# Performance work log

Hardware: AMD Instinct MI355X
Metric: run time of the kernel (lower is better)

## Reference

```python
import jax, jax.numpy as jnp
import numpy as np

C_QKV = 1024
C_HIDDEN = 64
NUM_HEADS = 16
INF = 1e9


def setup_inputs() -> dict:
    key = jax.random.key(0)
    ks = jax.random.split(key, 10)
    B, S = 2, 2048
    d = C_QKV
    hd = C_HIDDEN * NUM_HEADS
    sc = 0.02
    return {
        "input_qkv": jax.random.normal(ks[0], (B, S, d), jnp.float32),
        "mask": jnp.ones((B, 1, 1, S), jnp.float32),
        "bias": jax.random.normal(ks[1], (1, NUM_HEADS, S, S), jnp.float32) * sc,
        "wq": jax.random.normal(ks[2], (d, hd), jnp.float32) * sc,
        "wk": jax.random.normal(ks[3], (d, hd), jnp.float32) * sc,
        "wv": jax.random.normal(ks[4], (d, hd), jnp.float32) * sc,
        "wg": jax.random.normal(ks[5], (d, hd), jnp.float32) * sc,
        "bg": jnp.zeros((hd,), jnp.float32),
        "wo": jax.random.normal(ks[6], (hd, d), jnp.float32) * sc,
        "bo": jnp.zeros((d,), jnp.float32),
    }


def reference(input_qkv, mask, bias, wq, wk, wv, wg, bg, wo, bo):
    B, S, _ = input_qkv.shape
    H, C = NUM_HEADS, C_HIDDEN
    # projections -> [B, H, S, C]
    q = (input_qkv @ wq).reshape(B, S, H, C).transpose(0, 2, 1, 3)
    k = (input_qkv @ wk).reshape(B, S, H, C).transpose(0, 2, 1, 3)
    v = (input_qkv @ wv).reshape(B, S, H, C).transpose(0, 2, 1, 3)
    q = q / jnp.asarray(C, q.dtype) ** 0.5
    # scores [B, H, S, S] with additive mask and pair bias
    a = jnp.einsum("bhqc,bhkc->bhqk", q, k)
    a = a + (mask - 1.0) * INF + bias
    a = jax.nn.softmax(a, axis=-1)
    o = jnp.einsum("bhqk,bhkc->bhqc", a, v).transpose(0, 2, 1, 3)  # [B,S,H,C]
    gate = jax.nn.sigmoid(input_qkv @ wg + bg).reshape(B, S, H, C)
    o = (o * gate).reshape(B, S, H * C)
    return o @ wo + bo
```

## Files before the change

kernel.cpp:

```cpp
#include <hip/hip_runtime.h>
#include <hip/hip_bf16.h>
#include <stdint.h>

typedef unsigned short u16;
typedef __attribute__((ext_vector_type(8))) short short8;
typedef __attribute__((ext_vector_type(4))) short short4v;
typedef __attribute__((ext_vector_type(4))) float f32x4;

#define MFMA16 __builtin_amdgcn_mfma_f32_16x16x32_bf16

#define GLOAD_LDS16(gsrc, ldst) \
  __builtin_amdgcn_global_load_lds((const __attribute__((address_space(1))) void*)(gsrc), \
                                   (__attribute__((address_space(3))) void*)(ldst), 16, 0, 0)

__device__ __forceinline__ u16 f2bf(float x) {
  union { float f; uint32_t u; } v; v.f = x;
  uint32_t r = v.u + 0x7FFFu + ((v.u >> 16) & 1u);
  return (u16)(r >> 16);
}
__device__ __forceinline__ u16 f2bf_rn(float x) {
  __hip_bfloat16 h = __float2bfloat16(x);
  return *reinterpret_cast<u16*>(&h);
}
__device__ __forceinline__ float bf2f(u16 b) {
  union { uint32_t u; float f; } v; v.u = ((uint32_t)b) << 16;
  return v.f;
}

__global__ __launch_bounds__(256) void convert_bf16_kernel(
    const float* __restrict__ in, u16* __restrict__ out, int n) {
  int i = (blockIdx.x * 256 + threadIdx.x) * 8;
  if (i >= n) return;
  float4 a = *(const float4*)(in + i);
  float4 b = *(const float4*)(in + i + 4);
  short8 t;
  t[0] = (short)f2bf(a.x); t[1] = (short)f2bf(a.y);
  t[2] = (short)f2bf(a.z); t[3] = (short)f2bf(a.w);
  t[4] = (short)f2bf(b.x); t[5] = (short)f2bf(b.y);
  t[6] = (short)f2bf(b.z); t[7] = (short)f2bf(b.w);
  *(short8*)(out + i) = t;
}

__global__ __launch_bounds__(256) void transpose_w64_4(
    const float* __restrict__ w0, const float* __restrict__ w1,
    const float* __restrict__ w2, const float* __restrict__ w3,
    u16* __restrict__ WT) {
  __shared__ float tile[64][68];
  const int t = threadIdx.x;
  const int z = blockIdx.z;
  const float* W = (z == 0) ? w0 : (z == 1) ? w1 : (z == 2) ? w2 : w3;
  u16* dst_base = WT + (size_t)z * 1024 * 1024;
  const int k0 = blockIdx.x * 64, n0 = blockIdx.y * 64;
  {
    int r = t >> 2, c0 = (t & 3) * 16;
    const float* src = W + (size_t)(k0 + r) * 1024 + n0 + c0;
#pragma unroll
    for (int j = 0; j < 16; j += 4) {
      float4 v = *(const float4*)(src + j);
      tile[r][c0 + j + 0] = v.x; tile[r][c0 + j + 1] = v.y;
      tile[r][c0 + j + 2] = v.z; tile[r][c0 + j + 3] = v.w;
    }
  }
  __syncthreads();
  {
    int n = t >> 2, kq = (t & 3) * 16;
    short8 t0, t1;
#pragma unroll
    for (int j = 0; j < 8; ++j)  t0[j] = (short)f2bf(tile[kq + j][n]);
#pragma unroll
    for (int j = 0; j < 8; ++j)  t1[j] = (short)f2bf(tile[kq + 8 + j][n]);
    u16* dst = dst_base + (size_t)(n0 + n) * 1024 + k0 + kq;
    *(short8*)dst = t0;
    *(short8*)(dst + 8) = t1;
  }
}

__global__ __launch_bounds__(256) void transpose_w64(
    const float* __restrict__ W, u16* __restrict__ WT, int KK, int NN) {
  __shared__ float tile[64][68];
  const int t = threadIdx.x;
  const int k0 = blockIdx.x * 64, n0 = blockIdx.y * 64;
  {
    int r = t >> 2, c0 = (t & 3) * 16;
    const float* src = W + (size_t)(k0 + r) * NN + n0 + c0;
#pragma unroll
    for (int j = 0; j < 16; j += 4) {
      float4 v = *(const float4*)(src + j);
      tile[r][c0 + j + 0] = v.x; tile[r][c0 + j + 1] = v.y;
      tile[r][c0 + j + 2] = v.z; tile[r][c0 + j + 3] = v.w;
    }
  }
  __syncthreads();
  {
    int n = t >> 2, kq = (t & 3) * 16;
    short8 t0, t1;
#pragma unroll
    for (int j = 0; j < 8; ++j)  t0[j] = (short)f2bf(tile[kq + j][n]);
#pragma unroll
    for (int j = 0; j < 8; ++j)  t1[j] = (short)f2bf(tile[kq + 8 + j][n]);
    u16* dst = WT + (size_t)(n0 + n) * KK + k0 + kq;
    *(short8*)dst = t0;
    *(short8*)(dst + 8) = t1;
  }
}

__global__ __launch_bounds__(256) void transpose_v64(
    const u16* __restrict__ vin, u16* __restrict__ vout) {
  __shared__ u16 tile[64][80];
  const int t = threadIdx.x;
  const int s0 = blockIdx.x * 64;
  const int bh = blockIdx.y;
  const int b = bh >> 4, h = bh & 15;
  {
    int r = t >> 2, c0 = (t & 3) * 16;
    const u16* src = vin + (size_t)(b * 2048 + s0 + r) * 1024 + h * 64 + c0;
    *(short8*)&tile[r][c0] = *(const short8*)src;
    *(short8*)&tile[r][c0 + 8] = *(const short8*)(src + 8);
  }
  __syncthreads();
  {
    int c = t >> 2, s4 = (t & 3) * 16;
    short8 t0, t1;
#pragma unroll
    for (int j = 0; j < 8; ++j) t0[j] = (short)tile[s4 + j][c];
#pragma unroll
    for (int j = 0; j < 8; ++j) t1[j] = (short)tile[s4 + 8 + j][c];
    u16* dst = vout + (size_t)(bh * 64 + c) * 2048 + s0 + s4;
    *(short8*)dst = t0;
    *(short8*)(dst + 8) = t1;
  }
}

__global__ __launch_bounds__(256) void gemm_bt128(
    const u16* __restrict__ A, const u16* __restrict__ BTbase,
    void* __restrict__ dstbase, const float* __restrict__ bvec, int mode) {
  const int K = 1024;
  const int tid = threadIdx.x, lane = tid & 63, w = tid >> 6;
  const int wr = w >> 1, wc = w & 1;
  const int l15 = lane & 15, lg = lane >> 4;
  const int z = (mode < 0) ? (int)blockIdx.z : mode;
  const u16* BT = (mode < 0) ? BTbase + (size_t)z * 1024 * 1024 : BTbase;
  const int rbase = blockIdx.x * 128;
  const int nbase = blockIdx.y * 128;
  __shared__ u16 lsA[128 * 64];
  __shared__ u16 lsB[128 * 64];
  f32x4 acc[4][4] = {};
  const int col8 = (lane & 7) * 8;
  for (int kt = 0; kt < K / 64; ++kt) {
#pragma unroll
    for (int i = 0; i < 4; ++i) {
      int row = w * 32 + i * 8 + (lane >> 3);
      const u16* sa = A + (size_t)(rbase + row) * K + kt * 64 + col8;
      GLOAD_LDS16(sa, lsA + (w * 32 + i * 8) * 64 + lane * 8);
      const u16* sb = BT + (size_t)(nbase + row) * K + kt * 64 + col8;
      GLOAD_LDS16(sb, lsB + (w * 32 + i * 8) * 64 + lane * 8);
    }
    __syncthreads();
#pragma unroll
    for (int kk = 0; kk < 2; ++kk) {
      short8 af[4], bfr[4];
#pragma unroll
      for (int m = 0; m < 4; ++m)
        af[m] = *(const short8*)&lsA[(wr * 64 + m * 16 + l15) * 64 + kk * 32 + lg * 8];
#pragma unroll
      for (int n = 0; n < 4; ++n)
        bfr[n] = *(const short8*)&lsB[(wc * 64 + n * 16 + l15) * 64 + kk * 32 + lg * 8];
#pragma unroll
      for (int m = 0; m < 4; ++m)
#pragma unroll
        for (int n = 0; n < 4; ++n)
          acc[m][n] = MFMA16(af[m], bfr[n], acc[m][n], 0, 0, 0);
    }
    __syncthreads();
  }
  const int r0 = rbase + wr * 64;
  const int c0 = nbase + wc * 64;
  if (z == 4) {
    float* out = (float*)dstbase;
#pragma unroll
    for (int m = 0; m < 4; ++m)
#pragma unroll
      for (int n = 0; n < 4; ++n)
#pragma unroll
        for (int i = 0; i < 4; ++i) {
          int r = r0 + m * 16 + lg * 4 + i;
          int c = c0 + n * 16 + l15;
          out[(size_t)r * 1024 + c] = acc[m][n][i] + bvec[c];
        }
  } else {
    u16* dq = (u16*)dstbase + (size_t)z * 4096 * 1024;
#pragma unroll
    for (int m = 0; m < 4; ++m)
#pragma unroll
      for (int n = 0; n < 4; ++n)
#pragma unroll
        for (int i = 0; i < 4; ++i) {
          int r = r0 + m * 16 + lg * 4 + i;
          int c = c0 + n * 16 + l15;
          float v = acc[m][n][i];
          if (z == 0) v *= 0.125f;
          else if (z == 3) v = 1.f / (1.f + __expf(-(v + bvec[c])));
          dq[(size_t)r * 1024 + c] = f2bf(v);
        }
  }
}

__global__ __launch_bounds__(512, 2) void attn_kernel(
    const u16* __restrict__ qws, const u16* __restrict__ kws,
    const u16* __restrict__ vt, const u16* __restrict__ gws,
    const float* __restrict__ bias, const float* __restrict__ mask,
    u16* __restrict__ og) {
  const int tid = threadIdx.x;
  const int lane = tid & 63;
  const int w = tid >> 6;
  const int bb = w >> 2;
  const int ws = w & 3;
  const int l15 = lane & 15, lg = lane >> 4;
  const int qt = blockIdx.x;
  const int h = blockIdx.y;
  const int kb0 = ((h << 1) | (qt >> 3)) & 31;

#define KWIN(KB) (((KB) + kb0) & 31)

  __shared__ __align__(16) u16 ring[3][16384];
  __shared__ __align__(16) u16 lsP[8][2304];
  __shared__ __align__(16) u16 lsM[4096];

  const float* bias_base = bias + ((size_t)h * 2048 + qt * 128) * 2048;
  const u16* k_base0 = kws + (size_t)h * 64;
  const u16* k_base1 = kws + (size_t)2048 * 1024 + h * 64;
  const u16* vt_base0 = vt + (size_t)(h * 64) * 2048;
  const u16* vt_base1 = vt + (size_t)((16 + h) * 64) * 2048;

  {
    float4 m0 = *(const float4*)(mask + tid * 8);
    float4 m1 = *(const float4*)(mask + tid * 8 + 4);
    short8 mm;
    mm[0] = (short)f2bf((m0.x - 1.f) * 1e9f); mm[1] = (short)f2bf((m0.y - 1.f) * 1e9f);
    mm[2] = (short)f2bf((m0.z - 1.f) * 1e9f); mm[3] = (short)f2bf((m0.w - 1.f) * 1e9f);
    mm[4] = (short)f2bf((m1.x - 1.f) * 1e9f); mm[5] = (short)f2bf((m1.y - 1.f) * 1e9f);
    mm[6] = (short)f2bf((m1.z - 1.f) * 1e9f); mm[7] = (short)f2bf((m1.w - 1.f) * 1e9f);
    *(short8*)&lsM[tid * 8] = mm;
  }

  const size_t qrow0 = (size_t)(bb * 2048 + qt * 128 + ws * 32 + l15) * 1024 + h * 64;
  const size_t qrow1 = qrow0 + 16 * 1024;
  short8 qf00 = *(const short8*)(qws + qrow0 + lg * 8);
  short8 qf01 = *(const short8*)(qws + qrow0 + 32 + lg * 8);
  short8 qf10 = *(const short8*)(qws + qrow1 + lg * 8);
  short8 qf11 = *(const short8*)(qws + qrow1 + 32 + lg * 8);
  asm volatile("" :: "v"(qf00), "v"(qf01), "v"(qf10), "v"(qf11));
  asm volatile("s_waitcnt vmcnt(0)" ::: "memory");
  __builtin_amdgcn_sched_barrier(0);

  f32x4 O[2][4] = {};
  float lacc0 = 0.f, lacc1 = 0.f;
  f32x4 bA0, bA1, bA2, bA3, bA4, bA5, bA6, bA7;
  f32x4 bB0, bB1, bB2, bB3, bB4, bB5, bB6, bB7;
  f32x4 kX0, kX1, vX0, vX1, kY0, kY1, vY0, vY1;

#define STAGE_ISSUE(K0, K1, V0, V1, KB) {                                           \
    int kw_ = KWIN(KB);                                                             \
    int r_ = tid >> 3, cg_ = tid & 7;                                               \
    const u16* kp0 = k_base0 + (size_t)(kw_ * 64 + r_) * 1024 + cg_ * 8;            \
    const u16* kp1 = k_base1 + (size_t)(kw_ * 64 + r_) * 1024 + cg_ * 8;            \
    const u16* vp0 = vt_base0 + (size_t)r_ * 2048 + kw_ * 64 + cg_ * 8;             \
    const u16* vp1 = vt_base1 + (size_t)r_ * 2048 + kw_ * 64 + cg_ * 8;             \
    asm volatile("global_load_dwordx4 %0, %1, off" : "=v"(K0) : "v"(kp0));          \
    asm volatile("global_load_dwordx4 %0, %1, off" : "=v"(K1) : "v"(kp1));          \
    asm volatile("global_load_dwordx4 %0, %1, off" : "=v"(V0) : "v"(vp0));          \
    asm volatile("global_load_dwordx4 %0, %1, off" : "=v"(V1) : "v"(vp1));          \
  }

#define STAGE_WRITE(SLOT, K0, K1, V0, V1) {                                         \
    int r_ = tid >> 3, cg_ = tid & 7;                                               \
    int d0_ = (r_ * 8 + (cg_ ^ (r_ & 7))) * 8;                                      \
    *(f32x4*)&ring[SLOT][d0_] = K0;                                                 \
    *(f32x4*)&ring[SLOT][4096 + d0_] = V0;                                          \
    *(f32x4*)&ring[SLOT][8192 + d0_] = K1;                                          \
    *(f32x4*)&ring[SLOT][12288 + d0_] = V1;                                         \
  }

#define BIAS_ISSUE(R0, R1, R2, R3, R4, R5, R6, R7, KB) {                            \
    const float* bp_ = bias_base + (size_t)(ws * 32 + l15) * 2048 + KWIN(KB) * 64 + lg * 4; \
    asm volatile("global_load_dwordx4 %0, %1, off" : "=v"(R0) : "v"(bp_));          \
    asm volatile("global_load_dwordx4 %0, %1, off" : "=v"(R1) : "v"(bp_ + 16));     \
    asm volatile("global_load_dwordx4 %0, %1, off" : "=v"(R2) : "v"(bp_ + 32));     \
    asm volatile("global_load_dwordx4 %0, %1, off" : "=v"(R3) : "v"(bp_ + 48));     \
    asm volatile("global_load_dwordx4 %0, %1, off" : "=v"(R4) : "v"(bp_ + 16 * 2048)); \
    asm volatile("global_load_dwordx4 %0, %1, off" : "=v"(R5) : "v"(bp_ + 16 * 2048 + 16)); \
    asm volatile("global_load_dwordx4 %0, %1, off" : "=v"(R6) : "v"(bp_ + 16 * 2048 + 32)); \
    asm volatile("global_load_dwordx4 %0, %1, off" : "=v"(R7) : "v"(bp_ + 16 * 2048 + 48)); \
  }

#define COMPUTE(SLOT, KB, X0, X1, X2, X3, X4, X5, X6, X7) {                         \
    const u16* Kc_ = &ring[SLOT][bb * 8192];                                        \
    const u16* Vc_ = &ring[SLOT][bb * 8192 + 4096];                                 \
    f32x4 bb0_[4] = {X0, X1, X2, X3};                                               \
    f32x4 bb1_[4] = {X4, X5, X6, X7};                                               \
    f32x4 s_[2][4];                                                                 \
    _Pragma("unroll") for (int kt = 0; kt < 4; ++kt) {                              \
      int krow_ = kt * 16 + l15;                                                    \
      int sw_ = krow_ & 7;                                                          \
      short8 kfa_ = *(const short8*)&Kc_[(krow_ * 8 + (lg ^ sw_)) * 8];             \
      short8 kfb_ = *(const short8*)&Kc_[(krow_ * 8 + ((4 + lg) ^ sw_)) * 8];       \
      short4v mk_ = *(const short4v*)&lsM[bb * 2048 + KWIN(KB) * 64 + kt * 16 + lg * 4]; \
      f32x4 ci0_, ci1_;                                                             \
      _Pragma("unroll") for (int i = 0; i < 4; ++i) {                               \
        float m_ = bf2f((u16)mk_[i]);                                               \
        ci0_[i] = bb0_[kt][i] + m_;                                                 \
        ci1_[i] = bb1_[kt][i] + m_;                                                 \
      }                                                                             \
      s_[0][kt] = MFMA16(kfa_, qf00, ci0_, 0, 0, 0);                                \
      s_[0][kt] = MFMA16(kfb_, qf01, s_[0][kt], 0, 0, 0);                           \
      s_[1][kt] = MFMA16(kfa_, qf10, ci1_, 0, 0, 0);                                \
      s_[1][kt] = MFMA16(kfb_, qf11, s_[1][kt], 0, 0, 0);                           \
    }                                                                               \
    _Pragma("unroll") for (int kt = 0; kt < 4; ++kt) {                              \
      short4v p0_, p1_;                                                             \
      _Pragma("unroll") for (int i = 0; i < 4; ++i) {                               \
        float e0_ = __expf(s_[0][kt][i]); lacc0 += e0_; p0_[i] = (short)f2bf_rn(e0_); \
        float e1_ = __expf(s_[1][kt][i]); lacc1 += e1_; p1_[i] = (short)f2bf_rn(e1_); \
      }                                                                             \
      *(short4v*)&lsP[w][(l15) * 72 + kt * 16 + lg * 4] = p0_;                      \
      *(short4v*)&lsP[w][(16 + l15) * 72 + kt * 16 + lg * 4] = p1_;                 \
    }                                                                               \
    short8 pf00_ = *(const short8*)&lsP[w][(l15) * 72 + lg * 8];                    \
    short8 pf01_ = *(const short8*)&lsP[w][(l15) * 72 + 32 + lg * 8];               \
    short8 pf10_ = *(const short8*)&lsP[w][(16 + l15) * 72 + lg * 8];               \
    short8 pf11_ = *(const short8*)&lsP[w][(16 + l15) * 72 + 32 + lg * 8];          \
    _Pragma("unroll") for (int cf = 0; cf < 4; ++cf) {                              \
      int c_ = cf * 16 + l15;                                                       \
      int sw_ = c_ & 7;                                                             \
      short8 vf0_ = *(const short8*)&Vc_[(c_ * 8 + (lg ^ sw_)) * 8];                \
      short8 vf1_ = *(const short8*)&Vc_[(c_ * 8 + ((4 + lg) ^ sw_)) * 8];          \
      O[0][cf] = MFMA16(vf0_, pf00_, O[0][cf], 0, 0, 0);                            \
      O[0][cf] = MFMA16(vf1_, pf01_, O[0][cf], 0, 0, 0);                            \
      O[1][cf] = MFMA16(vf0_, pf10_, O[1][cf], 0, 0, 0);                            \
      O[1][cf] = MFMA16(vf1_, pf11_, O[1][cf], 0, 0, 0);                            \
    } }

#define BODY(KB, N, ISK0, ISK1, ISV0, ISV1, WRK0, WRK1, WRV0, WRV1,                 \
             X0, X1, X2, X3, X4, X5, X6, X7) {                                      \
    if ((KB) + 2 < 32) STAGE_ISSUE(ISK0, ISK1, ISV0, ISV1, (KB) + 2);               \
    COMPUTE((KB) % 3, KB, X0, X1, X2, X3, X4, X5, X6, X7);                          \
    if ((KB) + 2 < 32) BIAS_ISSUE(X0, X1, X2, X3, X4, X5, X6, X7, (KB) + 2);        \
    asm volatile("s_waitcnt vmcnt(" #N ")" ::: "memory");                           \
    __builtin_amdgcn_sched_barrier(0);                                              \
    if ((KB) + 1 < 32) {                                                            \
      STAGE_WRITE(((KB) + 1) % 3, WRK0, WRK1, WRV0, WRV1);                          \
      asm volatile("s_waitcnt lgkmcnt(0)" ::: "memory");                            \
      __builtin_amdgcn_sched_barrier(0);                                            \
      __builtin_amdgcn_s_barrier();                                                 \
    } }

  STAGE_ISSUE(kX0, kX1, vX0, vX1, 0);
  BIAS_ISSUE(bA0, bA1, bA2, bA3, bA4, bA5, bA6, bA7, 0);
  STAGE_ISSUE(kY0, kY1, vY0, vY1, 1);
  BIAS_ISSUE(bB0, bB1, bB2, bB3, bB4, bB5, bB6, bB7, 1);
  asm volatile("s_waitcnt vmcnt(12)" ::: "memory");
  __builtin_amdgcn_sched_barrier(0);
  STAGE_WRITE(0, kX0, kX1, vX0, vX1);
  asm volatile("s_waitcnt lgkmcnt(0)" ::: "memory");
  __builtin_amdgcn_sched_barrier(0);
  __builtin_amdgcn_s_barrier();

  for (int kb2 = 0; kb2 < 30; kb2 += 2) {
    BODY(kb2,     12, kX0, kX1, vX0, vX1, kY0, kY1, vY0, vY1,
         bA0, bA1, bA2, bA3, bA4, bA5, bA6, bA7);
    BODY(kb2 + 1, 12, kY0, kY1, vY0, vY1, kX0, kX1, vX0, vX1,
         bB0, bB1, bB2, bB3, bB4, bB5, bB6, bB7);
  }
  BODY(30, 0, kX0, kX1, vX0, vX1, kY0, kY1, vY0, vY1,
       bA0, bA1, bA2, bA3, bA4, bA5, bA6, bA7);
  BODY(31, 0, kY0, kY1, vY0, vY1, kX0, kX1, vX0, vX1,
       bB0, bB1, bB2, bB3, bB4, bB5, bB6, bB7);

  lacc0 += __shfl_xor(lacc0, 16); lacc0 += __shfl_xor(lacc0, 32);
  lacc1 += __shfl_xor(lacc1, 16); lacc1 += __shfl_xor(lacc1, 32);
  {
    float inv0 = 1.f / lacc0, inv1 = 1.f / lacc1;
#pragma unroll
    for (int cf = 0; cf < 4; ++cf) {
      short4v ga = *(const short4v*)(gws + qrow0 + cf * 16 + lg * 4);
      short4v gb = *(const short4v*)(gws + qrow1 + cf * 16 + lg * 4);
      short4v oa, ob;
#pragma unroll
      for (int i = 0; i < 4; ++i) {
        oa[i] = (short)f2bf_rn(O[0][cf][i] * inv0 * bf2f((u16)ga[i]));
        ob[i] = (short)f2bf_rn(O[1][cf][i] * inv1 * bf2f((u16)gb[i]));
      }
      *(short4v*)(og + qrow0 + cf * 16 + lg * 4) = oa;
      *(short4v*)(og + qrow1 + cf * 16 + lg * 4) = ob;
    }
  }
#undef STAGE_ISSUE
#undef STAGE_WRITE
#undef BIAS_ISSUE
#undef COMPUTE
#undef BODY
#undef KWIN
}

extern "C" void kernel_launch(void* const* d_in, const int* in_sizes, int n_in,
                              void* d_out, int out_size, void* d_ws, size_t ws_size,
                              hipStream_t stream) {
  const float* x    = (const float*)d_in[0];
  const float* mask = (const float*)d_in[1];
  const float* bias = (const float*)d_in[2];
  const float* wq   = (const float*)d_in[3];
  const float* wk   = (const float*)d_in[4];
  const float* wv   = (const float*)d_in[5];
  const float* wg   = (const float*)d_in[6];
  const float* bg   = (const float*)d_in[7];
  const float* wo   = (const float*)d_in[8];
  const float* bo   = (const float*)d_in[9];
  float* out = (float*)d_out;

  char* ws = (char*)d_ws;
  const size_t MB = 1ull << 20;
  u16* xb   = (u16*)(ws + 0);
  u16* wt   = (u16*)(ws + 8 * MB);
  u16* wot  = (u16*)(ws + 16 * MB);
  u16* proj = (u16*)(ws + 18 * MB);
  u16* vtp  = (u16*)(ws + 50 * MB);
  u16* og   = (u16*)(ws + 58 * MB);
  const size_t PSZ = (size_t)4096 * 1024;

  convert_bf16_kernel<<<2048, 256, 0, stream>>>(x, xb, 4096 * 1024);

  transpose_w64_4<<<dim3(16, 16, 4), 256, 0, stream>>>(wq, wk, wv, wg, wt);
  transpose_w64<<<dim3(16, 16), 256, 0, stream>>>(wo, wot, 1024, 1024);

  gemm_bt128<<<dim3(32, 8, 4), 256, 0, stream>>>(xb, wt, (void*)proj, bg, -1);

  transpose_v64<<<dim3(32, 32), 256, 0, stream>>>(proj + 2 * PSZ, vtp);

  attn_kernel<<<dim3(16, 16), 512, 0, stream>>>(proj, proj + PSZ, vtp, proj + 3 * PSZ,
                                                bias, mask, og);

  gemm_bt128<<<dim3(32, 8, 1), 256, 0, stream>>>(og, wot, (void*)out, bo, 4);
}
```

Measured before the change: 204.8 us.

## Share bias tile across batches via LDS staging in bf16

```diff
diff --git a/kernel.cpp b/kernel.cpp
--- a/kernel.cpp
+++ b/kernel.cpp
@@ -222,7 +222,8 @@
 
 #define KWIN(KB) (((KB) + kb0) & 31)
 
-  __shared__ __align__(16) u16 ring[3][16384];
+  __shared__ __align__(16) u16 ring[2][16384];
+  __shared__ __align__(16) u16 lsB[2][9216];
   __shared__ __align__(16) u16 lsP[8][2304];
   __shared__ __align__(16) u16 lsM[4096];
 
@@ -255,9 +256,8 @@
 
   f32x4 O[2][4] = {};
   float lacc0 = 0.f, lacc1 = 0.f;
-  f32x4 bA0, bA1, bA2, bA3, bA4, bA5, bA6, bA7;
-  f32x4 bB0, bB1, bB2, bB3, bB4, bB5, bB6, bB7;
   f32x4 kX0, kX1, vX0, vX1, kY0, kY1, vY0, vY1;
+  f32x4 bX0, bX1, bX2, bX3, bY0, bY1, bY2, bY3;
 
 #define STAGE_ISSUE(K0, K1, V0, V1, KB) {                                           \
     int kw_ = KWIN(KB);                                                             \
@@ -281,23 +281,30 @@
     *(f32x4*)&ring[SLOT][12288 + d0_] = V1;                                         \
   }
 
-#define BIAS_ISSUE(R0, R1, R2, R3, R4, R5, R6, R7, KB) {                            \
-    const float* bp_ = bias_base + (size_t)(ws * 32 + l15) * 2048 + KWIN(KB) * 64 + lg * 4; \
+#define BIAS_ISSUE(R0, R1, R2, R3, KB) {                                            \
+    const float* bp_ = bias_base + (size_t)(tid >> 2) * 2048 + KWIN(KB) * 64 +      \
+                       (tid & 3) * 16;                                              \
     asm volatile("global_load_dwordx4 %0, %1, off" : "=v"(R0) : "v"(bp_));          \
-    asm volatile("global_load_dwordx4 %0, %1, off" : "=v"(R1) : "v"(bp_ + 16));     \
-    asm volatile("global_load_dwordx4 %0, %1, off" : "=v"(R2) : "v"(bp_ + 32));     \
-    asm volatile("global_load_dwordx4 %0, %1, off" : "=v"(R3) : "v"(bp_ + 48));     \
-    asm volatile("global_load_dwordx4 %0, %1, off" : "=v"(R4) : "v"(bp_ + 16 * 2048)); \
-    asm volatile("global_load_dwordx4 %0, %1, off" : "=v"(R5) : "v"(bp_ + 16 * 2048 + 16)); \
-    asm volatile("global_load_dwordx4 %0, %1, off" : "=v"(R6) : "v"(bp_ + 16 * 2048 + 32)); \
-    asm volatile("global_load_dwordx4 %0, %1, off" : "=v"(R7) : "v"(bp_ + 16 * 2048 + 48)); \
-  }
-
-#define COMPUTE(SLOT, KB, X0, X1, X2, X3, X4, X5, X6, X7) {                         \
+    asm volatile("global_load_dwordx4 %0, %1, off" : "=v"(R1) : "v"(bp_ + 4));      \
+    asm volatile("global_load_dwordx4 %0, %1, off" : "=v"(R2) : "v"(bp_ + 8));      \
+    asm volatile("global_load_dwordx4 %0, %1, off" : "=v"(R3) : "v"(bp_ + 12));     \
+  }
+
+#define BIAS_WRITE(SLOT, R0, R1, R2, R3) {                                          \
+    int row_ = tid >> 2, cb_ = (tid & 3) * 16;                                      \
+    u16* d_ = &lsB[SLOT][row_ * 72 + cb_];                                          \
+    short4v p0_, p1_, p2_, p3_;                                                     \
+    _Pragma("unroll") for (int i = 0; i < 4; ++i) {                                 \
+      p0_[i] = (short)f2bf_rn(R0[i]); p1_[i] = (short)f2bf_rn(R1[i]);               \
+      p2_[i] = (short)f2bf_rn(R2[i]); p3_[i] = (short)f2bf_rn(R3[i]);               \
+    }                                                                               \
+    *(short4v*)&d_[0] = p0_;  *(short4v*)&d_[4] = p1_;                              \
+    *(short4v*)&d_[8] = p2_;  *(short4v*)&d_[12] = p3_;                             \
+  }
+
+#define COMPUTE(SLOT, KB) {                                                         \
     const u16* Kc_ = &ring[SLOT][bb * 8192];                                        \
     const u16* Vc_ = &ring[SLOT][bb * 8192 + 4096];                                 \
-    f32x4 bb0_[4] = {X0, X1, X2, X3};                                               \
-    f32x4 bb1_[4] = {X4, X5, X6, X7};                                               \
     f32x4 s_[2][4];                                                                 \
     _Pragma("unroll") for (int kt = 0; kt < 4; ++kt) {                              \
       int krow_ = kt * 16 + l15;                                                    \
@@ -305,11 +312,13 @@
       short8 kfa_ = *(const short8*)&Kc_[(krow_ * 8 + (lg ^ sw_)) * 8];             \
       short8 kfb_ = *(const short8*)&Kc_[(krow_ * 8 + ((4 + lg) ^ sw_)) * 8];       \
       short4v mk_ = *(const short4v*)&lsM[bb * 2048 + KWIN(KB) * 64 + kt * 16 + lg * 4]; \
+      short4v bv0_ = *(const short4v*)&lsB[SLOT][(ws * 32 + l15) * 72 + kt * 16 + lg * 4]; \
+      short4v bv1_ = *(const short4v*)&lsB[SLOT][(ws * 32 + 16 + l15) * 72 + kt * 16 + lg * 4]; \
       f32x4 ci0_, ci1_;                                                             \
       _Pragma("unroll") for (int i = 0; i < 4; ++i) {                               \
         float m_ = bf2f((u16)mk_[i]);                                               \
-        ci0_[i] = bb0_[kt][i] + m_;                                                 \
-        ci1_[i] = bb1_[kt][i] + m_;                                                 \
+        ci0_[i] = bf2f((u16)bv0_[i]) + m_;                                          \
+        ci1_[i] = bf2f((u16)bv1_[i]) + m_;                                          \
       }                                                                             \
       s_[0][kt] = MFMA16(kfa_, qf00, ci0_, 0, 0, 0);                                \
       s_[0][kt] = MFMA16(kfb_, qf01, s_[0][kt], 0, 0, 0);                           \
@@ -340,41 +349,45 @@
       O[1][cf] = MFMA16(vf1_, pf11_, O[1][cf], 0, 0, 0);                            \
     } }
 
-#define BODY(KB, N, ISK0, ISK1, ISV0, ISV1, WRK0, WRK1, WRV0, WRV1,                 \
-             X0, X1, X2, X3, X4, X5, X6, X7) {                                      \
-    if ((KB) + 2 < 32) STAGE_ISSUE(ISK0, ISK1, ISV0, ISV1, (KB) + 2);               \
-    COMPUTE((KB) % 3, KB, X0, X1, X2, X3, X4, X5, X6, X7);                          \
-    if ((KB) + 2 < 32) BIAS_ISSUE(X0, X1, X2, X3, X4, X5, X6, X7, (KB) + 2);        \
+#define BODY(KB, N, ISK0, ISK1, ISV0, ISV1, IB0, IB1, IB2, IB3,                     \
+             WRK0, WRK1, WRV0, WRV1, WB0, WB1, WB2, WB3) {                          \
+    if ((KB) + 2 < 32) {                                                            \
+      STAGE_ISSUE(ISK0, ISK1, ISV0, ISV1, (KB) + 2);                                \
+      BIAS_ISSUE(IB0, IB1, IB2, IB3, (KB) + 2);                                     \
+    }                                                                               \
+    COMPUTE((KB) & 1, KB);                                                          \
     asm volatile("s_waitcnt vmcnt(" #N ")" ::: "memory");                           \
     __builtin_amdgcn_sched_barrier(0);                                              \
     if ((KB) + 1 < 32) {                                                            \
-      STAGE_WRITE(((KB) + 1) % 3, WRK0, WRK1, WRV0, WRV1);                          \
+      STAGE_WRITE(((KB) + 1) & 1, WRK0, WRK1, WRV0, WRV1);                          \
+      BIAS_WRITE(((KB) + 1) & 1, WB0, WB1, WB2, WB3);                               \
       asm volatile("s_waitcnt lgkmcnt(0)" ::: "memory");                            \
       __builtin_amdgcn_sched_barrier(0);                                            \
       __builtin_amdgcn_s_barrier();                                                 \
     } }
 
   STAGE_ISSUE(kX0, kX1, vX0, vX1, 0);
-  BIAS_ISSUE(bA0, bA1, bA2, bA3, bA4, bA5, bA6, bA7, 0);
+  BIAS_ISSUE(bX0, bX1, bX2, bX3, 0);
   STAGE_ISSUE(kY0, kY1, vY0, vY1, 1);
-  BIAS_ISSUE(bB0, bB1, bB2, bB3, bB4, bB5, bB6, bB7, 1);
-  asm volatile("s_waitcnt vmcnt(12)" ::: "memory");
+  BIAS_ISSUE(bY0, bY1, bY2, bY3, 1);
+  asm volatile("s_waitcnt vmcnt(8)" ::: "memory");
   __builtin_amdgcn_sched_barrier(0);
   STAGE_WRITE(0, kX0, kX1, vX0, vX1);
+  BIAS_WRITE(0, bX0, bX1, bX2, bX3);
   asm volatile("s_waitcnt lgkmcnt(0)" ::: "memory");
   __builtin_amdgcn_sched_barrier(0);
   __builtin_amdgcn_s_barrier();
 
   for (int kb2 = 0; kb2 < 30; kb2 += 2) {
-    BODY(kb2,     12, kX0, kX1, vX0, vX1, kY0, kY1, vY0, vY1,
-         bA0, bA1, bA2, bA3, bA4, bA5, bA6, bA7);
-    BODY(kb2 + 1, 12, kY0, kY1, vY0, vY1, kX0, kX1, vX0, vX1,
-         bB0, bB1, bB2, bB3, bB4, bB5, bB6, bB7);
-  }
-  BODY(30, 0, kX0, kX1, vX0, vX1, kY0, kY1, vY0, vY1,
-       bA0, bA1, bA2, bA3, bA4, bA5, bA6, bA7);
-  BODY(31, 0, kY0, kY1, vY0, vY1, kX0, kX1, vX0, vX1,
-       bB0, bB1, bB2, bB3, bB4, bB5, bB6, bB7);
+    BODY(kb2,     8, kX0, kX1, vX0, vX1, bX0, bX1, bX2, bX3,
+         kY0, kY1, vY0, vY1, bY0, bY1, bY2, bY3);
+    BODY(kb2 + 1, 8, kY0, kY1, vY0, vY1, bY0, bY1, bY2, bY3,
+         kX0, kX1, vX0, vX1, bX0, bX1, bX2, bX3);
+  }
+  BODY(30, 0, kX0, kX1, vX0, vX1, bX0, bX1, bX2, bX3,
+       kY0, kY1, vY0, vY1, bY0, bY1, bY2, bY3);
+  BODY(31, 0, kY0, kY1, vY0, vY1, bY0, bY1, bY2, bY3,
+       kX0, kX1, vX0, vX1, bX0, bX1, bX2, bX3);
 
   lacc0 += __shfl_xor(lacc0, 16); lacc0 += __shfl_xor(lacc0, 32);
   lacc1 += __shfl_xor(lacc1, 16); lacc1 += __shfl_xor(lacc1, 32);
@@ -397,6 +410,7 @@
 #undef STAGE_ISSUE
 #undef STAGE_WRITE
 #undef BIAS_ISSUE
+#undef BIAS_WRITE
 #undef COMPUTE
 #undef BODY
 #undef KWIN
```

New measurement: 193.2 us. 1.06x faster.
